# Kernel optimization log

Hardware: AMD Instinct MI355X
Metric: run time of the kernel (lower is better)

The kernel has to match this reference:

```python
import jax, jax.numpy as jnp
import numpy as np

BN_EPS = 1e-5
N_OUT, D_OUT = 64, 128


def setup_inputs() -> dict:
    key = jax.random.key(0)
    k1, k2, k3, k4 = jax.random.split(key, 4)
    B, N_in, D_in, K = 512, 64, 128, 4
    x = jax.random.normal(k1, (B, N_in, D_in), dtype=jnp.float32)
    # block-sparse weights: one (D_in x D_out) block per (output-row, active-input-row) pair
    W = jax.random.normal(k2, (N_OUT, K, D_in, D_OUT), dtype=jnp.float32) * (1.0 / np.sqrt(K * D_in))
    bias = jax.random.normal(k3, (N_OUT, D_OUT), dtype=jnp.float32) * 0.02
    gamma = jnp.ones((N_OUT * D_OUT,), dtype=jnp.float32)
    beta = jnp.zeros((N_OUT * D_OUT,), dtype=jnp.float32)
    idx = jax.random.randint(k4, (N_OUT, K), 0, N_in, dtype=jnp.int32)
    return {"x": x, "W": W, "bias": bias, "gamma": gamma, "beta": beta, "idx": idx}


def reference(x, W, bias, gamma, beta, idx):
    B = x.shape[0]
    # structured-sparse linear: gather active input rows, per-block matmul
    xg = x[:, idx, :]                                   # [B, N_out, K, D_in]
    y = jnp.einsum('bokd,okde->boe', xg, W) + bias      # [B, N_out, D_out]
    # BatchNorm1d (training-mode batch statistics) on flattened features
    yf = y.reshape(B, -1)                               # [B, N_out*D_out]
    mean = jnp.mean(yf, axis=0)
    var = jnp.mean(jnp.square(yf - mean), axis=0)       # biased variance, as in torch BN
    yn = (yf - mean) * jax.lax.rsqrt(var + BN_EPS) * gamma + beta
    # Swish: z * sigmoid(z)
    out = yn * jax.nn.sigmoid(yn)
    return out.reshape(B, N_OUT, D_OUT)
```

## Files before the change

### kernel.cpp

```cpp
#include <hip/hip_runtime.h>


typedef __attribute__((ext_vector_type(8))) __bf16 bf16x8;
typedef __attribute__((ext_vector_type(4))) float  f32x4;

#define FEAT 8192
#define XROW 8192
#define LDSB 520

__global__ __launch_bounds__(1024, 4)
void fused_encoder(const float* __restrict__ x, const float* __restrict__ W,
                   const float* __restrict__ bias, const float* __restrict__ gamma,
                   const float* __restrict__ beta, const int* __restrict__ idxp,
                   float* __restrict__ out)
{
    __shared__ __bf16 Bpan[32 * LDSB];
    __shared__ float Sred[16][32];
    __shared__ float Qred[16][32];
    __shared__ float sscale[32];
    __shared__ float sshift[32];

    const int bid = blockIdx.x;
    const int o   = ((bid >> 5) << 3) | (bid & 7);
    const int es  = (bid >> 3) & 3;
    const int e0  = es * 32;

    const int tid  = threadIdx.x;
    const int wave = tid >> 6;
    const int lane = tid & 63;
    const int lam  = lane & 15;
    const int quad = lane >> 4;

    int rsel[4];
#pragma unroll
    for (int k = 0; k < 4; ++k) rsel[k] = idxp[o * 4 + k];

    {
        const int e  = tid & 31;
        const int k0 = (tid >> 5) * 16;
        float v[16];
#pragma unroll
        for (int j = 0; j < 16; ++j) {
            const int k = k0 + j;
            v[j] = W[(((o * 4 + (k >> 7)) * 128) + (k & 127)) * 128 + e0 + e];
        }
        bf16x8 w0, w1;
#pragma unroll
        for (int j = 0; j < 8; ++j) {
            w0[j] = (__bf16)v[j];
            w1[j] = (__bf16)v[8 + j];
        }
        *(bf16x8*)&Bpan[e * LDSB + k0]     = w0;
        *(bf16x8*)&Bpan[e * LDSB + k0 + 8] = w1;
    }

    const f32x4 zero4 = {0.f, 0.f, 0.f, 0.f};
    f32x4 acc[2][2];
#pragma unroll
    for (int mi = 0; mi < 2; ++mi)
#pragma unroll
        for (int ni = 0; ni < 2; ++ni) acc[mi][ni] = zero4;

    const float* xrow0 = x + (wave * 32 + lam)      * XROW;
    const float* xrow1 = x + (wave * 32 + 16 + lam) * XROW;

    f32x4 sa0[4], sa1[4];

    auto loadA = [&](f32x4 (&SA)[4], const int kkc) {
        const int r  = rsel[kkc >> 2];
        const int dd = (kkc & 3) * 32 + quad * 8;
        const float* p0 = xrow0 + r * 128 + dd;
        const float* p1 = xrow1 + r * 128 + dd;
        SA[0] = *(const f32x4*)(p0);
        SA[1] = *(const f32x4*)(p0 + 4);
        SA[2] = *(const f32x4*)(p1);
        SA[3] = *(const f32x4*)(p1 + 4);
    };
    auto cvtA = [&](const f32x4 (&SA)[4], bf16x8 (&af)[2]) {
#pragma unroll
        for (int j = 0; j < 4; ++j) {
            af[0][j]     = (__bf16)SA[0][j];
            af[0][j + 4] = (__bf16)SA[1][j];
            af[1][j]     = (__bf16)SA[2][j];
            af[1][j + 4] = (__bf16)SA[3][j];
        }
    };

    loadA(sa0, 0);
    loadA(sa1, 1);
    __syncthreads();

#pragma unroll
    for (int kk = 0; kk < 16; ++kk) {
        bf16x8 af[2];
        if ((kk & 1) == 0) {
            cvtA(sa0, af);
            if (kk + 2 < 16) loadA(sa0, kk + 2);
        } else {
            cvtA(sa1, af);
            if (kk + 2 < 16) loadA(sa1, kk + 2);
        }
        const bf16x8 b0 = *(const bf16x8*)&Bpan[lam        * LDSB + kk * 32 + quad * 8];
        const bf16x8 b1 = *(const bf16x8*)&Bpan[(16 + lam) * LDSB + kk * 32 + quad * 8];
        acc[0][0] = __builtin_amdgcn_mfma_f32_16x16x32_bf16(af[0], b0, acc[0][0], 0, 0, 0);
        acc[0][1] = __builtin_amdgcn_mfma_f32_16x16x32_bf16(af[0], b1, acc[0][1], 0, 0, 0);
        acc[1][0] = __builtin_amdgcn_mfma_f32_16x16x32_bf16(af[1], b0, acc[1][0], 0, 0, 0);
        acc[1][1] = __builtin_amdgcn_mfma_f32_16x16x32_bf16(af[1], b1, acc[1][1], 0, 0, 0);
    }

    float bvals[2];
#pragma unroll
    for (int ni = 0; ni < 2; ++ni)
        bvals[ni] = bias[o * 128 + e0 + ni * 16 + lam];
#pragma unroll
    for (int mi = 0; mi < 2; ++mi)
#pragma unroll
        for (int ni = 0; ni < 2; ++ni)
#pragma unroll
            for (int rr = 0; rr < 4; ++rr) acc[mi][ni][rr] += bvals[ni];

#pragma unroll
    for (int ni = 0; ni < 2; ++ni) {
        float s = 0.f, q = 0.f;
#pragma unroll
        for (int mi = 0; mi < 2; ++mi)
#pragma unroll
            for (int rr = 0; rr < 4; ++rr) {
                const float v = acc[mi][ni][rr];
                s += v; q += v * v;
            }
        s += __shfl_xor(s, 16); s += __shfl_xor(s, 32);
        q += __shfl_xor(q, 16); q += __shfl_xor(q, 32);
        if (quad == 0) {
            Sred[wave][ni * 16 + lam] = s;
            Qred[wave][ni * 16 + lam] = q;
        }
    }
    __syncthreads();

    if (tid < 32) {
        float s = 0.f, q = 0.f;
#pragma unroll
        for (int w = 0; w < 16; ++w) {
            s += Sred[w][tid];
            q += Qred[w][tid];
        }
        const float mean = s * (1.0f / 512.0f);
        const float var  = q * (1.0f / 512.0f) - mean * mean;
        const float rstd = rsqrtf(var + 1e-5f);
        const float sc   = rstd * gamma[o * 128 + e0 + tid];
        sscale[tid] = sc;
        sshift[tid] = beta[o * 128 + e0 + tid] - mean * sc;
    }
    __syncthreads();

#pragma unroll
    for (int mi = 0; mi < 2; ++mi) {
        const int rowb = wave * 32 + mi * 16 + quad * 4;
#pragma unroll
        for (int ni = 0; ni < 2; ++ni) {
            const int col = ni * 16 + lam;
            const float sc = sscale[col];
            const float sh = sshift[col];
#pragma unroll
            for (int rr = 0; rr < 4; ++rr) {
                const float xn = acc[mi][ni][rr] * sc + sh;
                const float sg = 1.0f / (1.0f + __expf(-xn));
                out[(rowb + rr) * FEAT + o * 128 + e0 + col] = xn * sg;
            }
        }
    }
}

extern "C" void kernel_launch(void* const* d_in, const int* in_sizes, int n_in,
                              void* d_out, int out_size, void* d_ws, size_t ws_size,
                              hipStream_t stream)
{
    const float* x     = (const float*)d_in[0];
    const float* W     = (const float*)d_in[1];
    const float* bias  = (const float*)d_in[2];
    const float* gamma = (const float*)d_in[3];
    const float* beta  = (const float*)d_in[4];
    const int*   idx   = (const int*)d_in[5];
    float* out = (float*)d_out;

    fused_encoder<<<dim3(256), dim3(1024), 0, stream>>>(
        x, W, bias, gamma, beta, idx, out);
}
```

Baseline: 115.6 us.

## Pre-convert x and W to bf16 in a separate pass before the fused GEMM

Adds a grid-stride kernel that converts the full x and W tensors from fp32 to bf16 into workspace before the main kernel runs. The fused encoder then gathers bf16 rows directly and feeds them to MFMA without per-iteration conversions. This halves the bytes moved by the heavily repeated x gathers across blocks and removes conversion ALU work from the inner loop. In exchange it adds a second launch and a full extra read and write pass over both inputs, plus a dependency between the two kernels.

```diff
diff --git a/kernel.cpp b/kernel.cpp
--- a/kernel.cpp
+++ b/kernel.cpp
@@ -7,9 +7,34 @@
 #define FEAT 8192
 #define XROW 8192
 #define LDSB 520
+#define NX8  524288
+#define NW8  524288
+
+__global__ __launch_bounds__(256)
+void cvt_kernel(const float* __restrict__ x, const float* __restrict__ W,
+                __bf16* __restrict__ xb, __bf16* __restrict__ wb)
+{
+    const int stride = gridDim.x * blockDim.x;
+    for (int i = blockIdx.x * blockDim.x + threadIdx.x; i < NX8 + NW8; i += stride) {
+        const float* src;
+        __bf16* dst;
+        int c;
+        if (i < NX8) { src = x; dst = xb; c = i; }
+        else         { src = W; dst = wb; c = i - NX8; }
+        const f32x4 v0 = *(const f32x4*)(src + c * 8);
+        const f32x4 v1 = *(const f32x4*)(src + c * 8 + 4);
+        bf16x8 o;
+#pragma unroll
+        for (int j = 0; j < 4; ++j) {
+            o[j]     = (__bf16)v0[j];
+            o[j + 4] = (__bf16)v1[j];
+        }
+        *(bf16x8*)(dst + c * 8) = o;
+    }
+}
 
 __global__ __launch_bounds__(1024, 4)
-void fused_encoder(const float* __restrict__ x, const float* __restrict__ W,
+void fused_encoder(const __bf16* __restrict__ xb, const __bf16* __restrict__ wb,
                    const float* __restrict__ bias, const float* __restrict__ gamma,
                    const float* __restrict__ beta, const int* __restrict__ idxp,
                    float* __restrict__ out)
@@ -38,17 +63,12 @@
     {
         const int e  = tid & 31;
         const int k0 = (tid >> 5) * 16;
-        float v[16];
-#pragma unroll
-        for (int j = 0; j < 16; ++j) {
-            const int k = k0 + j;
-            v[j] = W[(((o * 4 + (k >> 7)) * 128) + (k & 127)) * 128 + e0 + e];
-        }
         bf16x8 w0, w1;
 #pragma unroll
         for (int j = 0; j < 8; ++j) {
-            w0[j] = (__bf16)v[j];
-            w1[j] = (__bf16)v[8 + j];
+            const int ka = k0 + j, kb = k0 + 8 + j;
+            w0[j] = wb[(((o * 4 + (ka >> 7)) * 128) + (ka & 127)) * 128 + e0 + e];
+            w1[j] = wb[(((o * 4 + (kb >> 7)) * 128) + (kb & 127)) * 128 + e0 + e];
         }
         *(bf16x8*)&Bpan[e * LDSB + k0]     = w0;
         *(bf16x8*)&Bpan[e * LDSB + k0 + 8] = w1;
@@ -61,51 +81,39 @@
 #pragma unroll
         for (int ni = 0; ni < 2; ++ni) acc[mi][ni] = zero4;
 
-    const float* xrow0 = x + (wave * 32 + lam)      * XROW;
-    const float* xrow1 = x + (wave * 32 + 16 + lam) * XROW;
-
-    f32x4 sa0[4], sa1[4];
-
-    auto loadA = [&](f32x4 (&SA)[4], const int kkc) {
+    const __bf16* xrow0 = xb + (wave * 32 + lam)      * XROW;
+    const __bf16* xrow1 = xb + (wave * 32 + 16 + lam) * XROW;
+
+    bf16x8 a0f0, a0f1, a1f0, a1f1;
+
+    auto loadA = [&](bf16x8& F0, bf16x8& F1, const int kkc) {
         const int r  = rsel[kkc >> 2];
         const int dd = (kkc & 3) * 32 + quad * 8;
-        const float* p0 = xrow0 + r * 128 + dd;
-        const float* p1 = xrow1 + r * 128 + dd;
-        SA[0] = *(const f32x4*)(p0);
-        SA[1] = *(const f32x4*)(p0 + 4);
-        SA[2] = *(const f32x4*)(p1);
-        SA[3] = *(const f32x4*)(p1 + 4);
+        F0 = *(const bf16x8*)(xrow0 + r * 128 + dd);
+        F1 = *(const bf16x8*)(xrow1 + r * 128 + dd);
     };
-    auto cvtA = [&](const f32x4 (&SA)[4], bf16x8 (&af)[2]) {
-#pragma unroll
-        for (int j = 0; j < 4; ++j) {
-            af[0][j]     = (__bf16)SA[0][j];
-            af[0][j + 4] = (__bf16)SA[1][j];
-            af[1][j]     = (__bf16)SA[2][j];
-            af[1][j + 4] = (__bf16)SA[3][j];
-        }
-    };
-
-    loadA(sa0, 0);
-    loadA(sa1, 1);
+
+    loadA(a0f0, a0f1, 0);
+    loadA(a1f0, a1f1, 1);
     __syncthreads();
 
 #pragma unroll
     for (int kk = 0; kk < 16; ++kk) {
-        bf16x8 af[2];
-        if ((kk & 1) == 0) {
-            cvtA(sa0, af);
-            if (kk + 2 < 16) loadA(sa0, kk + 2);
-        } else {
-            cvtA(sa1, af);
-            if (kk + 2 < 16) loadA(sa1, kk + 2);
-        }
         const bf16x8 b0 = *(const bf16x8*)&Bpan[lam        * LDSB + kk * 32 + quad * 8];
         const bf16x8 b1 = *(const bf16x8*)&Bpan[(16 + lam) * LDSB + kk * 32 + quad * 8];
-        acc[0][0] = __builtin_amdgcn_mfma_f32_16x16x32_bf16(af[0], b0, acc[0][0], 0, 0, 0);
-        acc[0][1] = __builtin_amdgcn_mfma_f32_16x16x32_bf16(af[0], b1, acc[0][1], 0, 0, 0);
-        acc[1][0] = __builtin_amdgcn_mfma_f32_16x16x32_bf16(af[1], b0, acc[1][0], 0, 0, 0);
-        acc[1][1] = __builtin_amdgcn_mfma_f32_16x16x32_bf16(af[1], b1, acc[1][1], 0, 0, 0);
+        if ((kk & 1) == 0) {
+            acc[0][0] = __builtin_amdgcn_mfma_f32_16x16x32_bf16(a0f0, b0, acc[0][0], 0, 0, 0);
+            acc[0][1] = __builtin_amdgcn_mfma_f32_16x16x32_bf16(a0f0, b1, acc[0][1], 0, 0, 0);
+            acc[1][0] = __builtin_amdgcn_mfma_f32_16x16x32_bf16(a0f1, b0, acc[1][0], 0, 0, 0);
+            acc[1][1] = __builtin_amdgcn_mfma_f32_16x16x32_bf16(a0f1, b1, acc[1][1], 0, 0, 0);
+            if (kk + 2 < 16) loadA(a0f0, a0f1, kk + 2);
+        } else {
+            acc[0][0] = __builtin_amdgcn_mfma_f32_16x16x32_bf16(a1f0, b0, acc[0][0], 0, 0, 0);
+            acc[0][1] = __builtin_amdgcn_mfma_f32_16x16x32_bf16(a1f0, b1, acc[0][1], 0, 0, 0);
+            acc[1][0] = __builtin_amdgcn_mfma_f32_16x16x32_bf16(a1f1, b0, acc[1][0], 0, 0, 0);
+            acc[1][1] = __builtin_amdgcn_mfma_f32_16x16x32_bf16(a1f1, b1, acc[1][1], 0, 0, 0);
+            if (kk + 2 < 16) loadA(a1f0, a1f1, kk + 2);
+        }
     }
 
     float bvals[2];
@@ -184,6 +192,10 @@
     const int*   idx   = (const int*)d_in[5];
     float* out = (float*)d_out;
 
+    __bf16* xb = (__bf16*)d_ws;
+    __bf16* wbp = xb + (size_t)NX8 * 8;
+
+    cvt_kernel<<<dim3(1024), dim3(256), 0, stream>>>(x, W, xb, wbp);
     fused_encoder<<<dim3(256), dim3(1024), 0, stream>>>(
-        x, W, bias, gamma, beta, idx, out);
+        xb, wbp, bias, gamma, beta, idx, out);
 }
```

New measurement: 110.0 us. -4.8%, faster.

## Pre-convert x to bf16 in workspace and deepen the A-operand prefetch pipeline

Applied to the files above, without the earlier changes.

Adds a separate kernel that converts x from fp32 to bf16 into the workspace buffer. The main kernel then gathers bf16 rows, halving the bytes each block reads for the repeatedly gathered x rows. It also issues six stages of A loads before the W panel staging and double-buffers the B fragments read from LDS. The cost is an extra launch plus a full read of x and a write of its bf16 copy, and the deeper prefetch raises register pressure.

```diff
diff --git a/kernel.cpp b/kernel.cpp
--- a/kernel.cpp
+++ b/kernel.cpp
@@ -7,9 +7,28 @@
 #define FEAT 8192
 #define XROW 8192
 #define LDSB 520
+#define NX8  524288
+#define ADEPTH 6
+
+__global__ __launch_bounds__(256)
+void cvt_kernel(const float* __restrict__ x, __bf16* __restrict__ xb)
+{
+    const int stride = gridDim.x * blockDim.x;
+    for (int c = blockIdx.x * blockDim.x + threadIdx.x; c < NX8; c += stride) {
+        const f32x4 v0 = *(const f32x4*)(x + c * 8);
+        const f32x4 v1 = *(const f32x4*)(x + c * 8 + 4);
+        bf16x8 o;
+#pragma unroll
+        for (int j = 0; j < 4; ++j) {
+            o[j]     = (__bf16)v0[j];
+            o[j + 4] = (__bf16)v1[j];
+        }
+        *(bf16x8*)(xb + c * 8) = o;
+    }
+}
 
 __global__ __launch_bounds__(1024, 4)
-void fused_encoder(const float* __restrict__ x, const float* __restrict__ W,
+void fused_encoder(const __bf16* __restrict__ xb, const float* __restrict__ W,
                    const float* __restrict__ bias, const float* __restrict__ gamma,
                    const float* __restrict__ beta, const int* __restrict__ idxp,
                    float* __restrict__ out)
@@ -35,6 +54,21 @@
 #pragma unroll
     for (int k = 0; k < 4; ++k) rsel[k] = idxp[o * 4 + k];
 
+    const __bf16* xrow0 = xb + (wave * 32 + lam)      * XROW;
+    const __bf16* xrow1 = xb + (wave * 32 + 16 + lam) * XROW;
+
+    bf16x8 sa[ADEPTH][2];
+
+    auto loadA = [&](const int stg, const int kkc) {
+        const int r  = rsel[kkc >> 2];
+        const int dd = (kkc & 3) * 32 + quad * 8;
+        sa[stg][0] = *(const bf16x8*)(xrow0 + r * 128 + dd);
+        sa[stg][1] = *(const bf16x8*)(xrow1 + r * 128 + dd);
+    };
+
+#pragma unroll
+    for (int p = 0; p < ADEPTH; ++p) loadA(p, p);
+
     {
         const int e  = tid & 31;
         const int k0 = (tid >> 5) * 16;
@@ -61,51 +95,25 @@
 #pragma unroll
         for (int ni = 0; ni < 2; ++ni) acc[mi][ni] = zero4;
 
-    const float* xrow0 = x + (wave * 32 + lam)      * XROW;
-    const float* xrow1 = x + (wave * 32 + 16 + lam) * XROW;
-
-    f32x4 sa0[4], sa1[4];
-
-    auto loadA = [&](f32x4 (&SA)[4], const int kkc) {
-        const int r  = rsel[kkc >> 2];
-        const int dd = (kkc & 3) * 32 + quad * 8;
-        const float* p0 = xrow0 + r * 128 + dd;
-        const float* p1 = xrow1 + r * 128 + dd;
-        SA[0] = *(const f32x4*)(p0);
-        SA[1] = *(const f32x4*)(p0 + 4);
-        SA[2] = *(const f32x4*)(p1);
-        SA[3] = *(const f32x4*)(p1 + 4);
-    };
-    auto cvtA = [&](const f32x4 (&SA)[4], bf16x8 (&af)[2]) {
-#pragma unroll
-        for (int j = 0; j < 4; ++j) {
-            af[0][j]     = (__bf16)SA[0][j];
-            af[0][j + 4] = (__bf16)SA[1][j];
-            af[1][j]     = (__bf16)SA[2][j];
-            af[1][j + 4] = (__bf16)SA[3][j];
-        }
-    };
-
-    loadA(sa0, 0);
-    loadA(sa1, 1);
     __syncthreads();
 
+    bf16x8 bq[2][2];
+    bq[0][0] = *(const bf16x8*)&Bpan[lam        * LDSB + quad * 8];
+    bq[0][1] = *(const bf16x8*)&Bpan[(16 + lam) * LDSB + quad * 8];
+
 #pragma unroll
     for (int kk = 0; kk < 16; ++kk) {
-        bf16x8 af[2];
-        if ((kk & 1) == 0) {
-            cvtA(sa0, af);
-            if (kk + 2 < 16) loadA(sa0, kk + 2);
-        } else {
-            cvtA(sa1, af);
-            if (kk + 2 < 16) loadA(sa1, kk + 2);
-        }
-        const bf16x8 b0 = *(const bf16x8*)&Bpan[lam        * LDSB + kk * 32 + quad * 8];
-        const bf16x8 b1 = *(const bf16x8*)&Bpan[(16 + lam) * LDSB + kk * 32 + quad * 8];
-        acc[0][0] = __builtin_amdgcn_mfma_f32_16x16x32_bf16(af[0], b0, acc[0][0], 0, 0, 0);
-        acc[0][1] = __builtin_amdgcn_mfma_f32_16x16x32_bf16(af[0], b1, acc[0][1], 0, 0, 0);
-        acc[1][0] = __builtin_amdgcn_mfma_f32_16x16x32_bf16(af[1], b0, acc[1][0], 0, 0, 0);
-        acc[1][1] = __builtin_amdgcn_mfma_f32_16x16x32_bf16(af[1], b1, acc[1][1], 0, 0, 0);
+        const int cur = kk & 1;
+        const int stg = kk % ADEPTH;
+        if (kk + 1 < 16) {
+            bq[cur ^ 1][0] = *(const bf16x8*)&Bpan[lam        * LDSB + (kk + 1) * 32 + quad * 8];
+            bq[cur ^ 1][1] = *(const bf16x8*)&Bpan[(16 + lam) * LDSB + (kk + 1) * 32 + quad * 8];
+        }
+        acc[0][0] = __builtin_amdgcn_mfma_f32_16x16x32_bf16(sa[stg][0], bq[cur][0], acc[0][0], 0, 0, 0);
+        acc[0][1] = __builtin_amdgcn_mfma_f32_16x16x32_bf16(sa[stg][0], bq[cur][1], acc[0][1], 0, 0, 0);
+        acc[1][0] = __builtin_amdgcn_mfma_f32_16x16x32_bf16(sa[stg][1], bq[cur][0], acc[1][0], 0, 0, 0);
+        acc[1][1] = __builtin_amdgcn_mfma_f32_16x16x32_bf16(sa[stg][1], bq[cur][1], acc[1][1], 0, 0, 0);
+        if (kk + ADEPTH < 16) loadA(stg, kk + ADEPTH);
     }
 
     float bvals[2];
@@ -184,6 +192,9 @@
     const int*   idx   = (const int*)d_in[5];
     float* out = (float*)d_out;
 
+    __bf16* xb = (__bf16*)d_ws;
+
+    cvt_kernel<<<dim3(512), dim3(256), 0, stream>>>(x, xb);
     fused_encoder<<<dim3(256), dim3(1024), 0, stream>>>(
-        x, W, bias, gamma, beta, idx, out);
+        xb, W, bias, gamma, beta, idx, out);
 }
```

Measured after the change: 106.2 us. 8.1% less time.
